# Kernel optimization log

Hardware: AMD Instinct MI355X
Metric: run time of the kernel (lower is better)

## Reference

```python
import jax, jax.numpy as jnp
import numpy as np

B, DIN, H, DOUT, RANK = 256, 128, 512, 1, 8
ALPHA = 16.0
SCALE = ALPHA / RANK  # LoRA scaling alpha/rank


def setup_inputs() -> dict:
    key = jax.random.key(0)
    keys = iter(jax.random.split(key, 64))

    def nrm(shape, s=0.05):
        return jax.random.normal(next(keys), shape, dtype=jnp.float32) * s

    inp = {"x": nrm((B, DIN), 1.0)}
    for i in range(3):
        inp[f"Wx{i}"] = nrm((H, DIN))
        inp[f"b{i}"] = jnp.zeros((H,), jnp.float32)
        inp[f"Ax{i}"] = nrm((B, RANK, DIN))
        inp[f"Bx{i}"] = nrm((B, H, RANK))
        inp[f"bd{i}"] = nrm((B, H))
    for i in (1, 2):
        inp[f"Wz{i}"] = nrm((H, H))
        inp[f"Az{i}"] = nrm((B, RANK, H))
        inp[f"Bz{i}"] = nrm((B, H, RANK))
    inp["out_Wx"] = nrm((DOUT, DIN))
    inp["out_b"] = jnp.zeros((DOUT,), jnp.float32)
    inp["out_Ax"] = nrm((B, RANK, DIN))
    inp["out_Bx"] = nrm((B, DOUT, RANK))
    inp["out_bd"] = nrm((B, DOUT))
    inp["out_Wz"] = nrm((DOUT, H))
    inp["out_Az"] = nrm((B, RANK, H))
    inp["out_Bz"] = nrm((B, DOUT, RANK))
    return inp


def _delta(Bm, Am):
    # per-sample LoRA delta: bmm(B, A) * alpha/rank -> [B, out, in]
    return jnp.einsum('bor,bri->boi', Bm, Am) * SCALE


def _blin(v, W, b=None):
    # batched linear with per-sample weight W [B,out,in] applied to v [B,in]
    y = jnp.einsum('boi,bi->bo', W, v)
    return y if b is None else y + b


def reference(x, Wx0, b0, Ax0, Bx0, bd0, Wx1, b1, Ax1, Bx1, bd1,
              Wx2, b2, Ax2, Bx2, bd2, Wz1, Az1, Bz1, Wz2, Az2, Bz2,
              out_Wx, out_b, out_Ax, out_Bx, out_bd, out_Wz, out_Az, out_Bz):
    sp = jax.nn.softplus
    # layer 0
    z = sp(_blin(x, Wx0 + _delta(Bx0, Ax0), b0 + bd0))
    # layer 1: x path + positive (softplus) z path
    pre = _blin(x, Wx1 + _delta(Bx1, Ax1), b1 + bd1)
    pre = pre + _blin(z, sp(Wz1 + _delta(Bz1, Az1)))
    z = sp(pre)
    # layer 2
    pre = _blin(x, Wx2 + _delta(Bx2, Ax2), b2 + bd2)
    pre = pre + _blin(z, sp(Wz2 + _delta(Bz2, Az2)))
    z = sp(pre)
    # output layer
    out = _blin(x, out_Wx + _delta(out_Bx, out_Ax), out_b + out_bd)
    out = out + _blin(z, sp(out_Wz + _delta(out_Bz, out_Az)))
    return out
```

## Files before the change

kernel.cpp:

```cpp
#include <hip/hip_runtime.h>

#define NB    256
#define DIN   128
#define HH    512
#define RANK  8
#define SCALE 2.0f
#define LN2   0.69314718f
#define C192  5.2083335e-3f

#define WS_Z0   0
#define WS_P1   131072
#define WS_P2   262144
#define WS_END  393216

typedef float v2f __attribute__((ext_vector_type(2)));
typedef _Float16 h4v __attribute__((ext_vector_type(4)));

__device__ __forceinline__ v2f mk2(float a, float b) { v2f r; r.x = a; r.y = b; return r; }

__device__ __forceinline__ v2f pk_fma(v2f a, v2f b, v2f c) {
    v2f d; asm("v_pk_fma_f32 %0, %1, %2, %3" : "=v"(d) : "v"(a), "v"(b), "v"(c)); return d;
}
__device__ __forceinline__ v2f pk_mul(v2f a, v2f b) {
    v2f d; asm("v_pk_mul_f32 %0, %1, %2" : "=v"(d) : "v"(a), "v"(b)); return d;
}
__device__ __forceinline__ v2f pk_fma_blo(v2f a, v2f b, v2f c) {
    v2f d; asm("v_pk_fma_f32 %0, %1, %2, %3 op_sel:[0,0,0] op_sel_hi:[1,0,1]"
               : "=v"(d) : "v"(a), "v"(b), "v"(c)); return d;
}
__device__ __forceinline__ v2f pk_fma_bhi(v2f a, v2f b, v2f c) {
    v2f d; asm("v_pk_fma_f32 %0, %1, %2, %3 op_sel:[0,1,0] op_sel_hi:[1,1,1]"
               : "=v"(d) : "v"(a), "v"(b), "v"(c)); return d;
}

__device__ __forceinline__ float sp_stable(float v) {
    float e = __expf(-fabsf(v));
    return fmaxf(v, 0.0f) + __logf(1.0f + e);
}
__device__ __forceinline__ float sp_poly(float v) {
    float u = v * v;
    float t = fmaf(u, -C192, 0.125f);
    t = fmaf(u, t, LN2);
    return fmaf(v, 0.5f, t);
}

#define DPP_ADD(x, ctrl, rm, bm, bc)                                            \
    (x) = (x) + __int_as_float(__builtin_amdgcn_update_dpp(                     \
              0, __float_as_int(x), (ctrl), (rm), (bm), (bc)))

__device__ __forceinline__ float wave_sum64(float x) {
    DPP_ADD(x, 0x111, 0xf, 0xf, true);
    DPP_ADD(x, 0x112, 0xf, 0xf, true);
    DPP_ADD(x, 0x114, 0xf, 0xf, true);
    DPP_ADD(x, 0x118, 0xf, 0xf, true);
    DPP_ADD(x, 0x142, 0xa, 0xf, false);
    DPP_ADD(x, 0x143, 0xc, 0xf, false);
    return x;
}

__global__ __launch_bounds__(1024, 4) void kzstep(
    const float* __restrict__ x,
    const float* __restrict__ Wx, const float* __restrict__ bb,
    const float* __restrict__ Ax, const float* __restrict__ Bx,
    const float* __restrict__ bd,
    const float* __restrict__ Wz, const float* __restrict__ Az,
    const float* __restrict__ Bz,
    const float* __restrict__ zin, float* __restrict__ outv, const int mode)
{
    const int bid  = blockIdx.x;
    const int o    = bid >> 3;
    const int g    = bid & 7;
    const int tid  = threadIdx.x;
    const int lane = tid & 63;
    const int wid  = tid >> 6;

    __shared__ float x_s[8][DIN + 4];
    __shared__ float tx_s[8][RANK];
    __shared__ float xpre_s[64][9];
    __shared__ float z_s[8][HH];
    __shared__ _Float16 Wt[64 * HH];
    __shared__ float bz_s[8][64][RANK];
    __shared__ float red_s[4][8][2][65];

    const v2f cA2 = mk2(-C192, -C192);
    const v2f cB2 = mk2(0.125f, 0.125f);
    const v2f cL2 = mk2(LN2, LN2);
    const v2f cH2 = mk2(0.5f, 0.5f);

    {
        const int s = tid >> 7, d = tid & 127;
        x_s[s][d] = x[(o * 8 + s) * DIN + d];
    }
    if (mode) {
        {
            const int s = tid >> 7, k4 = tid & 127;
            float4 zv = *reinterpret_cast<const float4*>(zin + ((size_t)(o * 8 + s)) * HH + k4 * 4);
            if (mode == 2) {
                zv.x = sp_stable(zv.x); zv.y = sp_stable(zv.y);
                zv.z = sp_stable(zv.z); zv.w = sp_stable(zv.w);
            }
            *reinterpret_cast<float4*>(&z_s[s][k4 * 4]) = zv;
        }
        {
            #pragma unroll
            for (int j = 0; j < 8; ++j) {
                const int fi  = tid + j * 1024;
                const int row = fi >> 7, c4 = fi & 127;
                float4 w = *reinterpret_cast<const float4*>(Wz + (g * 64 + row) * HH + c4 * 4);
                h4v hv;
                hv.x = (_Float16)w.x; hv.y = (_Float16)w.y;
                hv.z = (_Float16)w.z; hv.w = (_Float16)w.w;
                reinterpret_cast<h4v*>(Wt)[fi] = hv;
            }
        }
        {
            const int s = tid >> 7, t2 = tid & 127;
            const int rw = t2 >> 1, q = t2 & 1;
            *reinterpret_cast<float4*>(&bz_s[s][rw][q * 4]) =
                *reinterpret_cast<const float4*>(
                    Bz + ((size_t)(o * 8 + s) * HH + g * 64 + rw) * RANK + q * 4);
        }
    }
    __syncthreads();

    if (tid < 512) {
        const int p = tid >> 3, l = tid & 7;
        const int s = p >> 3, r = p & 7;
        const float* Ab = Ax + ((size_t)(o * 8 + s) * RANK + r) * DIN;
        float acc = 0.f;
        #pragma unroll
        for (int j = 0; j < 16; ++j) { const int d = l + 8 * j; acc += Ab[d] * x_s[s][d]; }
        acc += __shfl_down(acc, 4, 8);
        acc += __shfl_down(acc, 2, 8);
        acc += __shfl_down(acc, 1, 8);
        if (l == 0) tx_s[s][r] = acc;
    }
    __syncthreads();

    if (tid < 512) {
        const int row = tid >> 3, s = tid & 7;
        const int h  = g * 64 + row;
        const int sb = o * 8 + s;
        const float4* wrow = reinterpret_cast<const float4*>(Wx + h * DIN);
        float acc = 0.f;
        #pragma unroll 8
        for (int q = 0; q < DIN / 4; ++q) {
            float4 w = wrow[q];
            const float* xs = &x_s[s][q * 4];
            acc += w.x * xs[0] + w.y * xs[1] + w.z * xs[2] + w.w * xs[3];
        }
        const float* bxr = Bx + ((size_t)sb * HH + h) * RANK;
        float t = 0.f;
        #pragma unroll
        for (int r = 0; r < RANK; ++r) t += bxr[r] * tx_s[s][r];
        const float v = acc + SCALE * t + bb[h] + bd[(size_t)sb * HH + h];
        if (mode == 0) outv[(size_t)sb * HH + h] = sp_stable(v);
        else           xpre_s[row][s] = v;
    }
    if (mode == 0) return;

    {
        const int s   = wid >> 1;
        const int khf = wid & 1;
        const int c0  = khf * 256 + (lane << 2);
        const int sb  = o * 8 + s;
        const bool odd = lane & 1;

        v2f zk2[2], az[RANK][2];
        {
            float4 zz = *reinterpret_cast<const float4*>(&z_s[s][c0]);
            zk2[0] = mk2(zz.x, zz.y); zk2[1] = mk2(zz.z, zz.w);
        }
        #pragma unroll
        for (int r = 0; r < RANK; ++r) {
            float4 a4 = *reinterpret_cast<const float4*>(Az + ((size_t)sb * RANK + r) * HH + c0);
            az[r][0] = mk2(SCALE * a4.x, SCALE * a4.y);
            az[r][1] = mk2(SCALE * a4.z, SCALE * a4.w);
        }

        const _Float16* wp = Wt + c0;
        v2f wA[2], wB[2], bzA[4], bzB[4];

        auto loadw = [&](v2f* dst, int row) {
            h4v hv = *reinterpret_cast<const h4v*>(wp + row * HH);
            dst[0] = mk2((float)hv.x, (float)hv.y);
            dst[1] = mk2((float)hv.z, (float)hv.w);
        };
        auto loadb = [&](v2f* dst, int row) {
            float4 q0 = *reinterpret_cast<const float4*>(&bz_s[s][row][0]);
            float4 q1 = *reinterpret_cast<const float4*>(&bz_s[s][row][4]);
            dst[0] = mk2(q0.x, q0.y); dst[1] = mk2(q0.z, q0.w);
            dst[2] = mk2(q1.x, q1.y); dst[3] = mk2(q1.z, q1.w);
        };
        auto rowsum = [&](const v2f* wz, const v2f* bz) -> float {
            v2f sv = mk2(0.f, 0.f);
            #pragma unroll
            for (int gg = 0; gg < 2; ++gg) {
                v2f d = wz[gg];
                d = pk_fma_blo(az[0][gg], bz[0], d);
                d = pk_fma_bhi(az[1][gg], bz[0], d);
                d = pk_fma_blo(az[2][gg], bz[1], d);
                d = pk_fma_bhi(az[3][gg], bz[1], d);
                d = pk_fma_blo(az[4][gg], bz[2], d);
                d = pk_fma_bhi(az[5][gg], bz[2], d);
                d = pk_fma_blo(az[6][gg], bz[3], d);
                d = pk_fma_bhi(az[7][gg], bz[3], d);
                v2f u = pk_mul(d, d);
                v2f t = pk_fma(u, cA2, cB2);
                t = pk_fma(u, t, cL2);
                t = pk_fma(d, cH2, t);
                sv = pk_fma(zk2[gg], t, sv);
            }
            return sv.x + sv.y;
        };

        loadw(wA, 0); loadb(bzA, 0);
        #pragma unroll 1
        for (int hs = 0; hs < 64; hs += 2) {
            loadw(wB, hs + 1); loadb(bzB, hs + 1);
            float sA = rowsum(wA, bzA);
            const int hn = (hs + 2) & 63;
            loadw(wA, hn); loadb(bzA, hn);
            float sB = rowsum(wB, bzB);

            float m  = odd ? sB : sA;
            float o2 = odd ? sA : sB;
            m = m + __int_as_float(__builtin_amdgcn_update_dpp(
                    0, __float_as_int(o2), 0xB1, 0xf, 0xf, true));
            DPP_ADD(m, 0x112, 0xf, 0xf, true);
            DPP_ADD(m, 0x114, 0xf, 0xf, true);
            DPP_ADD(m, 0x118, 0xf, 0xf, true);
            if ((lane & 14) == 14) red_s[lane >> 4][s][khf][hs + (lane & 1)] = m;
        }
    }
    __syncthreads();

    if (tid < 512) {
        const int row = tid >> 3, s = tid & 7;
        float acc = xpre_s[row][s];
        #pragma unroll
        for (int q = 0; q < 4; ++q)
            acc += red_s[q][s][0][row] + red_s[q][s][1][row];
        outv[((size_t)(o * 8 + s)) * HH + g * 64 + row] = acc;
    }
}

__global__ __launch_bounds__(512, 2) void kout(
    const float* __restrict__ x,
    const float* __restrict__ oWx, const float* __restrict__ ob,
    const float* __restrict__ oAx, const float* __restrict__ oBx, const float* __restrict__ obd,
    const float* __restrict__ oWz, const float* __restrict__ oAz, const float* __restrict__ oBz,
    const float* __restrict__ pre2, float* __restrict__ out)
{
    const int b = blockIdx.x, tid = threadIdx.x;
    __shared__ float x_s[DIN];
    __shared__ float red_s[HH];
    __shared__ float tx_s[RANK];

    if (tid < DIN) x_s[tid] = x[b * DIN + tid];
    __syncthreads();

    float partial;
    {
        const int h = tid;
        const float z2 = sp_stable(pre2[(size_t)b * HH + h]);
        float d = 0.f;
        #pragma unroll
        for (int r = 0; r < RANK; ++r)
            d = fmaf(oBz[b * RANK + r], oAz[((size_t)b * RANK + r) * HH + h], d);
        partial = z2 * sp_poly(fmaf(SCALE, d, oWz[h]));
        if (tid < DIN) partial += oWx[tid] * x_s[tid];
    }
    red_s[tid] = partial;
    __syncthreads();

    if (tid < 128) {
        const int r = tid >> 4, l = tid & 15;
        const float* Ab = oAx + ((size_t)b * RANK + r) * DIN;
        float s = 0.f;
        #pragma unroll
        for (int k = 0; k < 8; ++k) { int d = l + 16 * k; s += Ab[d] * x_s[d]; }
        s += __shfl_down(s, 8, 16);
        s += __shfl_down(s, 4, 16);
        s += __shfl_down(s, 2, 16);
        s += __shfl_down(s, 1, 16);
        if (l == 0) tx_s[r] = s;
    }
    __syncthreads();
    for (int st = 256; st > 0; st >>= 1) {
        if (tid < st) red_s[tid] += red_s[tid + st];
        __syncthreads();
    }
    if (tid == 0) {
        float t2 = 0.f;
        #pragma unroll
        for (int r = 0; r < RANK; ++r) t2 = fmaf(oBx[b * RANK + r], tx_s[r], t2);
        out[b] = red_s[0] + ob[0] + obd[b] + SCALE * t2;
    }
}

__global__ __launch_bounds__(1024, 4) void lora_fused(
    const float* __restrict__ x,
    const float* __restrict__ Wx0, const float* __restrict__ b0,
    const float* __restrict__ Ax0, const float* __restrict__ Bx0, const float* __restrict__ bd0,
    const float* __restrict__ Wx1, const float* __restrict__ b1,
    const float* __restrict__ Ax1, const float* __restrict__ Bx1, const float* __restrict__ bd1,
    const float* __restrict__ Wx2, const float* __restrict__ b2,
    const float* __restrict__ Ax2, const float* __restrict__ Bx2, const float* __restrict__ bd2,
    const float* __restrict__ Wz1, const float* __restrict__ Az1, const float* __restrict__ Bz1,
    const float* __restrict__ Wz2, const float* __restrict__ Az2, const float* __restrict__ Bz2,
    const float* __restrict__ oWx, const float* __restrict__ ob,
    const float* __restrict__ oAx, const float* __restrict__ oBx, const float* __restrict__ obd,
    const float* __restrict__ oWz, const float* __restrict__ oAz, const float* __restrict__ oBz,
    float* __restrict__ out)
{
    const int b    = blockIdx.x;
    const int tid  = threadIdx.x;
    const int lane = tid & 63;
    const int wid  = tid >> 6;
    const int rg   = wid >> 1;
    const int ch   = wid & 1;
    const bool odd = lane & 1;

    __shared__ float x_s[DIN];
    __shared__ float z_s[HH];
    __shared__ float tx_s[4][RANK];
    __shared__ float xpre_s[3][HH];
    __shared__ float red4_s[4][2][HH + 2];
    __shared__ __attribute__((aligned(16))) float Az_s[2][RANK * HH];
    __shared__ __attribute__((aligned(16))) float Bz_s[2][HH * RANK];
    __shared__ float red8[16];

    const v2f cA2 = mk2(-C192, -C192);
    const v2f cB2 = mk2(0.125f, 0.125f);
    const v2f cL2 = mk2(LN2, LN2);
    const v2f cH2 = mk2(0.5f, 0.5f);

    if (tid < DIN) x_s[tid] = x[b * DIN + tid];
    {
        const float4* a1 = reinterpret_cast<const float4*>(Az1 + b * RANK * HH);
        const float4* a2 = reinterpret_cast<const float4*>(Az2 + b * RANK * HH);
        const float4* z1 = reinterpret_cast<const float4*>(Bz1 + b * HH * RANK);
        const float4* z2 = reinterpret_cast<const float4*>(Bz2 + b * HH * RANK);
        reinterpret_cast<float4*>(Az_s[0])[tid] = a1[tid];
        reinterpret_cast<float4*>(Az_s[1])[tid] = a2[tid];
        reinterpret_cast<float4*>(Bz_s[0])[tid] = z1[tid];
        reinterpret_cast<float4*>(Bz_s[1])[tid] = z2[tid];
    }
    __syncthreads();

    if (tid < 512) {
        const int g = tid >> 7;
        const int t = tid & 127;
        const int r = t >> 4, l = t & 15;
        const float* A  = (g == 0) ? Ax0 : (g == 1) ? Ax1 : (g == 2) ? Ax2 : oAx;
        const float* Ab = A + (b * RANK + r) * DIN;
        float s = 0.f;
        #pragma unroll
        for (int k = 0; k < 8; ++k) { int d = l + 16 * k; s += Ab[d] * x_s[d]; }
        s += __shfl_down(s, 8, 16);
        s += __shfl_down(s, 4, 16);
        s += __shfl_down(s, 2, 16);
        s += __shfl_down(s, 1, 16);
        if (l == 0) tx_s[g][r] = s;
    }
    __syncthreads();

    #pragma unroll 1
    for (int idx = tid; idx < 3 * HH; idx += 1024) {
        const int l = idx >> 9;
        const int h = idx & (HH - 1);
        const float* Wxl = (l == 0) ? Wx0 : (l == 1) ? Wx1 : Wx2;
        const float* bl  = (l == 0) ? b0  : (l == 1) ? b1  : b2;
        const float* Bxl = (l == 0) ? Bx0 : (l == 1) ? Bx1 : Bx2;
        const float* bdl = (l == 0) ? bd0 : (l == 1) ? bd1 : bd2;
        const float4* wrow = reinterpret_cast<const float4*>(Wxl + h * DIN);
        float s = 0.f;
        #pragma unroll 8
        for (int q = 0; q < DIN / 4; ++q) {
            float4 w = wrow[q];
            const float* xs = &x_s[q * 4];
            s += w.x * xs[0] + w.y * xs[1] + w.z * xs[2] + w.w * xs[3];
        }
        const float* bxr = Bxl + (b * HH + h) * RANK;
        float t = 0.f;
        #pragma unroll
        for (int r = 0; r < RANK; ++r) t += bxr[r] * tx_s[l][r];
        xpre_s[l][h] = s + SCALE * t + bl[h] + bdl[b * HH + h];
    }
    __syncthreads();

    if (tid < HH) z_s[tid] = sp_stable(xpre_s[0][tid]);
    __syncthreads();

    auto zlayer = [&](const float* __restrict__ Wz, int li) {
        const int c0 = ch * 256 + (lane << 2);
        v2f zk2[2], az[RANK][2];
        {
            float4 zz = *reinterpret_cast<const float4*>(&z_s[c0]);
            zk2[0] = mk2(zz.x, zz.y); zk2[1] = mk2(zz.z, zz.w);
        }
        #pragma unroll
        for (int r = 0; r < RANK; ++r) {
            float4 a4 = *reinterpret_cast<const float4*>(&Az_s[li][r * HH + c0]);
            az[r][0] = mk2(SCALE * a4.x, SCALE * a4.y);
            az[r][1] = mk2(SCALE * a4.z, SCALE * a4.w);
        }
        const float* wp = Wz + (rg * 64) * HH + c0;
        const float* bp = &Bz_s[li][(rg * 64) * RANK];
        float* rp = &red4_s[lane >> 4][ch][rg * 64 + (lane & 1)];

        v2f wA[2], wB[2], bzA[4], bzB[4];
        auto loadw = [&](v2f* dst, int row) {
            float4 w4 = *reinterpret_cast<const float4*>(wp + row * HH);
            dst[0] = mk2(w4.x, w4.y); dst[1] = mk2(w4.z, w4.w);
        };
        auto loadb = [&](v2f* dst, int row) {
            const float4* q = reinterpret_cast<const float4*>(bp + row * RANK);
            float4 q0 = q[0], q1 = q[1];
            dst[0] = mk2(q0.x, q0.y); dst[1] = mk2(q0.z, q0.w);
            dst[2] = mk2(q1.x, q1.y); dst[3] = mk2(q1.z, q1.w);
        };
        auto rowsum = [&](const v2f* wz, const v2f* bz) -> float {
            v2f s = mk2(0.f, 0.f);
            #pragma unroll
            for (int g = 0; g < 2; ++g) {
                v2f d = wz[g];
                d = pk_fma_blo(az[0][g], bz[0], d);
                d = pk_fma_bhi(az[1][g], bz[0], d);
                d = pk_fma_blo(az[2][g], bz[1], d);
                d = pk_fma_bhi(az[3][g], bz[1], d);
                d = pk_fma_blo(az[4][g], bz[2], d);
                d = pk_fma_bhi(az[5][g], bz[2], d);
                d = pk_fma_blo(az[6][g], bz[3], d);
                d = pk_fma_bhi(az[7][g], bz[3], d);
                v2f u = pk_mul(d, d);
                v2f t = pk_fma(u, cA2, cB2);
                t = pk_fma(u, t, cL2);
                t = pk_fma(d, cH2, t);
                s = pk_fma(zk2[g], t, s);
            }
            return s.x + s.y;
        };

        loadw(wA, 0); loadb(bzA, 0);
        #pragma unroll 1
        for (int hs = 0; hs < 64; hs += 2) {
            loadw(wB, hs + 1); loadb(bzB, hs + 1);
            float sA = rowsum(wA, bzA);
            const int hn = (hs + 2) & 63;
            loadw(wA, hn); loadb(bzA, hn);
            float sB = rowsum(wB, bzB);
            float m = odd ? sB : sA;
            float o = odd ? sA : sB;
            m = m + __int_as_float(__builtin_amdgcn_update_dpp(
                    0, __float_as_int(o), 0xB1, 0xf, 0xf, true));
            DPP_ADD(m, 0x112, 0xf, 0xf, true);
            DPP_ADD(m, 0x114, 0xf, 0xf, true);
            DPP_ADD(m, 0x118, 0xf, 0xf, true);
            if ((lane & 14) == 14) rp[hs] = m;
        }
    };

    zlayer(Wz1, 0);
    __syncthreads();
    if (tid < HH) {
        float acc = xpre_s[1][tid];
        #pragma unroll
        for (int q = 0; q < 4; ++q) acc += red4_s[q][0][tid] + red4_s[q][1][tid];
        z_s[tid] = sp_stable(acc);
    }
    __syncthreads();

    zlayer(Wz2, 1);
    __syncthreads();
    if (tid < HH) {
        float acc = xpre_s[2][tid];
        #pragma unroll
        for (int q = 0; q < 4; ++q) acc += red4_s[q][0][tid] + red4_s[q][1][tid];
        z_s[tid] = sp_stable(acc);
    }
    __syncthreads();

    {
        float partial = 0.f;
        if (tid < HH) {
            const float* oBzb = oBz + b * RANK;
            const float* oAzb = oAz + b * RANK * HH;
            float d = 0.f;
            #pragma unroll
            for (int r = 0; r < RANK; ++r) d = fmaf(oBzb[r], oAzb[r * HH + tid], d);
            partial = z_s[tid] * sp_poly(fmaf(SCALE, d, oWz[tid]));
            if (tid < DIN) partial += oWx[tid] * x_s[tid];
        }
        partial = wave_sum64(partial);
        if (lane == 63) red8[wid] = partial;
        __syncthreads();
        if (tid == 0) {
            float t = 0.f;
            #pragma unroll
            for (int w = 0; w < 8; ++w) t += red8[w];
            float t2 = 0.f;
            const float* oBxb = oBx + b * RANK;
            #pragma unroll
            for (int r = 0; r < RANK; ++r) t2 = fmaf(oBxb[r], tx_s[3][r], t2);
            out[b] = t + ob[0] + obd[b] + SCALE * t2;
        }
    }
}

extern "C" void kernel_launch(void* const* d_in, const int* in_sizes, int n_in,
                              void* d_out, int out_size, void* d_ws, size_t ws_size,
                              hipStream_t stream) {
    const float* x   = (const float*)d_in[0];
    const float* Wx0 = (const float*)d_in[1];
    const float* b0  = (const float*)d_in[2];
    const float* Ax0 = (const float*)d_in[3];
    const float* Bx0 = (const float*)d_in[4];
    const float* bd0 = (const float*)d_in[5];
    const float* Wx1 = (const float*)d_in[6];
    const float* b1  = (const float*)d_in[7];
    const float* Ax1 = (const float*)d_in[8];
    const float* Bx1 = (const float*)d_in[9];
    const float* bd1 = (const float*)d_in[10];
    const float* Wx2 = (const float*)d_in[11];
    const float* b2  = (const float*)d_in[12];
    const float* Ax2 = (const float*)d_in[13];
    const float* Bx2 = (const float*)d_in[14];
    const float* bd2 = (const float*)d_in[15];
    const float* Wz1 = (const float*)d_in[16];
    const float* Az1 = (const float*)d_in[17];
    const float* Bz1 = (const float*)d_in[18];
    const float* Wz2 = (const float*)d_in[19];
    const float* Az2 = (const float*)d_in[20];
    const float* Bz2 = (const float*)d_in[21];
    const float* oWx = (const float*)d_in[22];
    const float* ob  = (const float*)d_in[23];
    const float* oAx = (const float*)d_in[24];
    const float* oBx = (const float*)d_in[25];
    const float* obd = (const float*)d_in[26];
    const float* oWz = (const float*)d_in[27];
    const float* oAz = (const float*)d_in[28];
    const float* oBz = (const float*)d_in[29];
    float* out = (float*)d_out;

    if (ws_size >= (size_t)WS_END * sizeof(float) && d_ws != nullptr) {
        float* ws = (float*)d_ws;
        kzstep<<<NB, 1024, 0, stream>>>(x, Wx0, b0, Ax0, Bx0, bd0,
                                        nullptr, nullptr, nullptr,
                                        nullptr, ws + WS_Z0, 0);
        kzstep<<<NB, 1024, 0, stream>>>(x, Wx1, b1, Ax1, Bx1, bd1,
                                        Wz1, Az1, Bz1,
                                        ws + WS_Z0, ws + WS_P1, 1);
        kzstep<<<NB, 1024, 0, stream>>>(x, Wx2, b2, Ax2, Bx2, bd2,
                                        Wz2, Az2, Bz2,
                                        ws + WS_P1, ws + WS_P2, 2);
        kout<<<NB, 512, 0, stream>>>(x, oWx, ob, oAx, oBx, obd,
                                     oWz, oAz, oBz, ws + WS_P2, out);
    } else {
        lora_fused<<<NB, 1024, 0, stream>>>(
            x, Wx0, b0, Ax0, Bx0, bd0, Wx1, b1, Ax1, Bx1, bd1,
            Wx2, b2, Ax2, Bx2, bd2, Wz1, Az1, Bz1, Wz2, Az2, Bz2,
            oWx, ob, oAx, oBx, obd, oWz, oAz, oBz, out);
    }
}
```

Measured before the change: 79.84 us.

## Always run the multi-kernel layer-split path using static device buffers

Removes the single-block-per-sample fused kernel and its workspace-size check. The three per-layer kzstep kernels and the kout kernel now always run, with their intermediate activations stored in statically allocated __device__ global arrays instead of the caller's workspace. Each kzstep block serves 8 samples on one 64-row slice, so the shared weight matrix is reused across samples rather than re-read once per sample. The cost is extra launches and global round-trips for the intermediates between layers.

```diff
diff --git a/kernel.cpp b/kernel.cpp
--- a/kernel.cpp
+++ b/kernel.cpp
@@ -8,10 +8,9 @@
 #define LN2   0.69314718f
 #define C192  5.2083335e-3f
 
-#define WS_Z0   0
-#define WS_P1   131072
-#define WS_P2   262144
-#define WS_END  393216
+__device__ float g_z0[NB * HH];
+__device__ float g_p1[NB * HH];
+__device__ float g_p2[NB * HH];
 
 typedef float v2f __attribute__((ext_vector_type(2)));
 typedef _Float16 h4v __attribute__((ext_vector_type(4)));
@@ -64,8 +63,7 @@
     const float* __restrict__ Ax, const float* __restrict__ Bx,
     const float* __restrict__ bd,
     const float* __restrict__ Wz, const float* __restrict__ Az,
-    const float* __restrict__ Bz,
-    const float* __restrict__ zin, float* __restrict__ outv, const int mode)
+    const float* __restrict__ Bz, const int mode)
 {
     const int bid  = blockIdx.x;
     const int o    = bid >> 3;
@@ -73,6 +71,9 @@
     const int tid  = threadIdx.x;
     const int lane = tid & 63;
     const int wid  = tid >> 6;
+
+    const float* zin = (mode == 1) ? g_z0 : g_p1;
+    float* outv = (mode == 0) ? g_z0 : (mode == 1) ? g_p1 : g_p2;
 
     __shared__ float x_s[8][DIN + 4];
     __shared__ float tx_s[8][RANK];
@@ -250,7 +251,7 @@
     const float* __restrict__ oWx, const float* __restrict__ ob,
     const float* __restrict__ oAx, const float* __restrict__ oBx, const float* __restrict__ obd,
     const float* __restrict__ oWz, const float* __restrict__ oAz, const float* __restrict__ oBz,
-    const float* __restrict__ pre2, float* __restrict__ out)
+    float* __restrict__ out)
 {
     const int b = blockIdx.x, tid = threadIdx.x;
     __shared__ float x_s[DIN];
@@ -263,7 +264,7 @@
     float partial;
     {
         const int h = tid;
-        const float z2 = sp_stable(pre2[(size_t)b * HH + h]);
+        const float z2 = sp_stable(g_p2[(size_t)b * HH + h]);
         float d = 0.f;
         #pragma unroll
         for (int r = 0; r < RANK; ++r)
@@ -296,216 +297,6 @@
         #pragma unroll
         for (int r = 0; r < RANK; ++r) t2 = fmaf(oBx[b * RANK + r], tx_s[r], t2);
         out[b] = red_s[0] + ob[0] + obd[b] + SCALE * t2;
-    }
-}
-
-__global__ __launch_bounds__(1024, 4) void lora_fused(
-    const float* __restrict__ x,
-    const float* __restrict__ Wx0, const float* __restrict__ b0,
-    const float* __restrict__ Ax0, const float* __restrict__ Bx0, const float* __restrict__ bd0,
-    const float* __restrict__ Wx1, const float* __restrict__ b1,
-    const float* __restrict__ Ax1, const float* __restrict__ Bx1, const float* __restrict__ bd1,
-    const float* __restrict__ Wx2, const float* __restrict__ b2,
-    const float* __restrict__ Ax2, const float* __restrict__ Bx2, const float* __restrict__ bd2,
-    const float* __restrict__ Wz1, const float* __restrict__ Az1, const float* __restrict__ Bz1,
-    const float* __restrict__ Wz2, const float* __restrict__ Az2, const float* __restrict__ Bz2,
-    const float* __restrict__ oWx, const float* __restrict__ ob,
-    const float* __restrict__ oAx, const float* __restrict__ oBx, const float* __restrict__ obd,
-    const float* __restrict__ oWz, const float* __restrict__ oAz, const float* __restrict__ oBz,
-    float* __restrict__ out)
-{
-    const int b    = blockIdx.x;
-    const int tid  = threadIdx.x;
-    const int lane = tid & 63;
-    const int wid  = tid >> 6;
-    const int rg   = wid >> 1;
-    const int ch   = wid & 1;
-    const bool odd = lane & 1;
-
-    __shared__ float x_s[DIN];
-    __shared__ float z_s[HH];
-    __shared__ float tx_s[4][RANK];
-    __shared__ float xpre_s[3][HH];
-    __shared__ float red4_s[4][2][HH + 2];
-    __shared__ __attribute__((aligned(16))) float Az_s[2][RANK * HH];
-    __shared__ __attribute__((aligned(16))) float Bz_s[2][HH * RANK];
-    __shared__ float red8[16];
-
-    const v2f cA2 = mk2(-C192, -C192);
-    const v2f cB2 = mk2(0.125f, 0.125f);
-    const v2f cL2 = mk2(LN2, LN2);
-    const v2f cH2 = mk2(0.5f, 0.5f);
-
-    if (tid < DIN) x_s[tid] = x[b * DIN + tid];
-    {
-        const float4* a1 = reinterpret_cast<const float4*>(Az1 + b * RANK * HH);
-        const float4* a2 = reinterpret_cast<const float4*>(Az2 + b * RANK * HH);
-        const float4* z1 = reinterpret_cast<const float4*>(Bz1 + b * HH * RANK);
-        const float4* z2 = reinterpret_cast<const float4*>(Bz2 + b * HH * RANK);
-        reinterpret_cast<float4*>(Az_s[0])[tid] = a1[tid];
-        reinterpret_cast<float4*>(Az_s[1])[tid] = a2[tid];
-        reinterpret_cast<float4*>(Bz_s[0])[tid] = z1[tid];
-        reinterpret_cast<float4*>(Bz_s[1])[tid] = z2[tid];
-    }
-    __syncthreads();
-
-    if (tid < 512) {
-        const int g = tid >> 7;
-        const int t = tid & 127;
-        const int r = t >> 4, l = t & 15;
-        const float* A  = (g == 0) ? Ax0 : (g == 1) ? Ax1 : (g == 2) ? Ax2 : oAx;
-        const float* Ab = A + (b * RANK + r) * DIN;
-        float s = 0.f;
-        #pragma unroll
-        for (int k = 0; k < 8; ++k) { int d = l + 16 * k; s += Ab[d] * x_s[d]; }
-        s += __shfl_down(s, 8, 16);
-        s += __shfl_down(s, 4, 16);
-        s += __shfl_down(s, 2, 16);
-        s += __shfl_down(s, 1, 16);
-        if (l == 0) tx_s[g][r] = s;
-    }
-    __syncthreads();
-
-    #pragma unroll 1
-    for (int idx = tid; idx < 3 * HH; idx += 1024) {
-        const int l = idx >> 9;
-        const int h = idx & (HH - 1);
-        const float* Wxl = (l == 0) ? Wx0 : (l == 1) ? Wx1 : Wx2;
-        const float* bl  = (l == 0) ? b0  : (l == 1) ? b1  : b2;
-        const float* Bxl = (l == 0) ? Bx0 : (l == 1) ? Bx1 : Bx2;
-        const float* bdl = (l == 0) ? bd0 : (l == 1) ? bd1 : bd2;
-        const float4* wrow = reinterpret_cast<const float4*>(Wxl + h * DIN);
-        float s = 0.f;
-        #pragma unroll 8
-        for (int q = 0; q < DIN / 4; ++q) {
-            float4 w = wrow[q];
-            const float* xs = &x_s[q * 4];
-            s += w.x * xs[0] + w.y * xs[1] + w.z * xs[2] + w.w * xs[3];
-        }
-        const float* bxr = Bxl + (b * HH + h) * RANK;
-        float t = 0.f;
-        #pragma unroll
-        for (int r = 0; r < RANK; ++r) t += bxr[r] * tx_s[l][r];
-        xpre_s[l][h] = s + SCALE * t + bl[h] + bdl[b * HH + h];
-    }
-    __syncthreads();
-
-    if (tid < HH) z_s[tid] = sp_stable(xpre_s[0][tid]);
-    __syncthreads();
-
-    auto zlayer = [&](const float* __restrict__ Wz, int li) {
-        const int c0 = ch * 256 + (lane << 2);
-        v2f zk2[2], az[RANK][2];
-        {
-            float4 zz = *reinterpret_cast<const float4*>(&z_s[c0]);
-            zk2[0] = mk2(zz.x, zz.y); zk2[1] = mk2(zz.z, zz.w);
-        }
-        #pragma unroll
-        for (int r = 0; r < RANK; ++r) {
-            float4 a4 = *reinterpret_cast<const float4*>(&Az_s[li][r * HH + c0]);
-            az[r][0] = mk2(SCALE * a4.x, SCALE * a4.y);
-            az[r][1] = mk2(SCALE * a4.z, SCALE * a4.w);
-        }
-        const float* wp = Wz + (rg * 64) * HH + c0;
-        const float* bp = &Bz_s[li][(rg * 64) * RANK];
-        float* rp = &red4_s[lane >> 4][ch][rg * 64 + (lane & 1)];
-
-        v2f wA[2], wB[2], bzA[4], bzB[4];
-        auto loadw = [&](v2f* dst, int row) {
-            float4 w4 = *reinterpret_cast<const float4*>(wp + row * HH);
-            dst[0] = mk2(w4.x, w4.y); dst[1] = mk2(w4.z, w4.w);
-        };
-        auto loadb = [&](v2f* dst, int row) {
-            const float4* q = reinterpret_cast<const float4*>(bp + row * RANK);
-            float4 q0 = q[0], q1 = q[1];
-            dst[0] = mk2(q0.x, q0.y); dst[1] = mk2(q0.z, q0.w);
-            dst[2] = mk2(q1.x, q1.y); dst[3] = mk2(q1.z, q1.w);
-        };
-        auto rowsum = [&](const v2f* wz, const v2f* bz) -> float {
-            v2f s = mk2(0.f, 0.f);
-            #pragma unroll
-            for (int g = 0; g < 2; ++g) {
-                v2f d = wz[g];
-                d = pk_fma_blo(az[0][g], bz[0], d);
-                d = pk_fma_bhi(az[1][g], bz[0], d);
-                d = pk_fma_blo(az[2][g], bz[1], d);
-                d = pk_fma_bhi(az[3][g], bz[1], d);
-                d = pk_fma_blo(az[4][g], bz[2], d);
-                d = pk_fma_bhi(az[5][g], bz[2], d);
-                d = pk_fma_blo(az[6][g], bz[3], d);
-                d = pk_fma_bhi(az[7][g], bz[3], d);
-                v2f u = pk_mul(d, d);
-                v2f t = pk_fma(u, cA2, cB2);
-                t = pk_fma(u, t, cL2);
-                t = pk_fma(d, cH2, t);
-                s = pk_fma(zk2[g], t, s);
-            }
-            return s.x + s.y;
-        };
-
-        loadw(wA, 0); loadb(bzA, 0);
-        #pragma unroll 1
-        for (int hs = 0; hs < 64; hs += 2) {
-            loadw(wB, hs + 1); loadb(bzB, hs + 1);
-            float sA = rowsum(wA, bzA);
-            const int hn = (hs + 2) & 63;
-            loadw(wA, hn); loadb(bzA, hn);
-            float sB = rowsum(wB, bzB);
-            float m = odd ? sB : sA;
-            float o = odd ? sA : sB;
-            m = m + __int_as_float(__builtin_amdgcn_update_dpp(
-                    0, __float_as_int(o), 0xB1, 0xf, 0xf, true));
-            DPP_ADD(m, 0x112, 0xf, 0xf, true);
-            DPP_ADD(m, 0x114, 0xf, 0xf, true);
-            DPP_ADD(m, 0x118, 0xf, 0xf, true);
-            if ((lane & 14) == 14) rp[hs] = m;
-        }
-    };
-
-    zlayer(Wz1, 0);
-    __syncthreads();
-    if (tid < HH) {
-        float acc = xpre_s[1][tid];
-        #pragma unroll
-        for (int q = 0; q < 4; ++q) acc += red4_s[q][0][tid] + red4_s[q][1][tid];
-        z_s[tid] = sp_stable(acc);
-    }
-    __syncthreads();
-
-    zlayer(Wz2, 1);
-    __syncthreads();
-    if (tid < HH) {
-        float acc = xpre_s[2][tid];
-        #pragma unroll
-        for (int q = 0; q < 4; ++q) acc += red4_s[q][0][tid] + red4_s[q][1][tid];
-        z_s[tid] = sp_stable(acc);
-    }
-    __syncthreads();
-
-    {
-        float partial = 0.f;
-        if (tid < HH) {
-            const float* oBzb = oBz + b * RANK;
-            const float* oAzb = oAz + b * RANK * HH;
-            float d = 0.f;
-            #pragma unroll
-            for (int r = 0; r < RANK; ++r) d = fmaf(oBzb[r], oAzb[r * HH + tid], d);
-            partial = z_s[tid] * sp_poly(fmaf(SCALE, d, oWz[tid]));
-            if (tid < DIN) partial += oWx[tid] * x_s[tid];
-        }
-        partial = wave_sum64(partial);
-        if (lane == 63) red8[wid] = partial;
-        __syncthreads();
-        if (tid == 0) {
-            float t = 0.f;
-            #pragma unroll
-            for (int w = 0; w < 8; ++w) t += red8[w];
-            float t2 = 0.f;
-            const float* oBxb = oBx + b * RANK;
-            #pragma unroll
-            for (int r = 0; r < RANK; ++r) t2 = fmaf(oBxb[r], tx_s[3][r], t2);
-            out[b] = t + ob[0] + obd[b] + SCALE * t2;
-        }
     }
 }
 
@@ -544,23 +335,12 @@
     const float* oBz = (const float*)d_in[29];
     float* out = (float*)d_out;
 
-    if (ws_size >= (size_t)WS_END * sizeof(float) && d_ws != nullptr) {
-        float* ws = (float*)d_ws;
-        kzstep<<<NB, 1024, 0, stream>>>(x, Wx0, b0, Ax0, Bx0, bd0,
-                                        nullptr, nullptr, nullptr,
-                                        nullptr, ws + WS_Z0, 0);
-        kzstep<<<NB, 1024, 0, stream>>>(x, Wx1, b1, Ax1, Bx1, bd1,
-                                        Wz1, Az1, Bz1,
-                                        ws + WS_Z0, ws + WS_P1, 1);
-        kzstep<<<NB, 1024, 0, stream>>>(x, Wx2, b2, Ax2, Bx2, bd2,
-                                        Wz2, Az2, Bz2,
-                                        ws + WS_P1, ws + WS_P2, 2);
-        kout<<<NB, 512, 0, stream>>>(x, oWx, ob, oAx, oBx, obd,
-                                     oWz, oAz, oBz, ws + WS_P2, out);
-    } else {
-        lora_fused<<<NB, 1024, 0, stream>>>(
-            x, Wx0, b0, Ax0, Bx0, bd0, Wx1, b1, Ax1, Bx1, bd1,
-            Wx2, b2, Ax2, Bx2, bd2, Wz1, Az1, Bz1, Wz2, Az2, Bz2,
-            oWx, ob, oAx, oBx, obd, oWz, oAz, oBz, out);
-    }
-}
+    kzstep<<<NB, 1024, 0, stream>>>(x, Wx0, b0, Ax0, Bx0, bd0,
+                                    nullptr, nullptr, nullptr, 0);
+    kzstep<<<NB, 1024, 0, stream>>>(x, Wx1, b1, Ax1, Bx1, bd1,
+                                    Wz1, Az1, Bz1, 1);
+    kzstep<<<NB, 1024, 0, stream>>>(x, Wx2, b2, Ax2, Bx2, bd2,
+                                    Wz2, Az2, Bz2, 2);
+    kout<<<NB, 512, 0, stream>>>(x, oWx, ob, oAx, oBx, obd,
+                                 oWz, oAz, oBz, out);
+}
```

After: 80.01 us. Within noise of the previous version (+0.2%).

## Hoist all x-path projections into a prep kernel and split z-steps finer

Applied to the files above, without the earlier changes.

Adds a kprep kernel that computes the x-path pre-activations for all three layers (with the layer-0 softplus applied) in one per-sample launch and writes them to workspace. The z-step kernel becomes 1024 blocks of 512 threads, each handling 2 samples and 64 output rows with the row range split across wave groups, replacing 256 blocks of 1024 threads over 8 samples. This is meant to cut per-layer serial x-projection work and raise parallelism, at the cost of reloading and converting Wz to fp16 in four times as many blocks. The fallback fused kernel's z loop is also restructured to keep an 8-row ring of W registers, but that path only runs when no workspace is available.

```diff
diff --git a/kernel.cpp b/kernel.cpp
--- a/kernel.cpp
+++ b/kernel.cpp
@@ -9,9 +9,11 @@
 #define C192  5.2083335e-3f
 
 #define WS_Z0   0
-#define WS_P1   131072
-#define WS_P2   262144
-#define WS_END  393216
+#define WS_XP1  131072
+#define WS_XP2  262144
+#define WS_P1   393216
+#define WS_P2   524288
+#define WS_END  655360
 
 typedef float v2f __attribute__((ext_vector_type(2)));
 typedef _Float16 h4v __attribute__((ext_vector_type(4)));
@@ -58,112 +60,123 @@
     return x;
 }
 
-__global__ __launch_bounds__(1024, 4) void kzstep(
+__global__ __launch_bounds__(1024, 4) void kprep(
     const float* __restrict__ x,
-    const float* __restrict__ Wx, const float* __restrict__ bb,
-    const float* __restrict__ Ax, const float* __restrict__ Bx,
-    const float* __restrict__ bd,
+    const float* __restrict__ Wx0, const float* __restrict__ b0,
+    const float* __restrict__ Ax0, const float* __restrict__ Bx0, const float* __restrict__ bd0,
+    const float* __restrict__ Wx1, const float* __restrict__ b1,
+    const float* __restrict__ Ax1, const float* __restrict__ Bx1, const float* __restrict__ bd1,
+    const float* __restrict__ Wx2, const float* __restrict__ b2,
+    const float* __restrict__ Ax2, const float* __restrict__ Bx2, const float* __restrict__ bd2,
+    float* __restrict__ ws)
+{
+    const int b = blockIdx.x, tid = threadIdx.x;
+    __shared__ float x_s[DIN];
+    __shared__ float tx_s[3][RANK];
+
+    if (tid < DIN) x_s[tid] = x[b * DIN + tid];
+    __syncthreads();
+
+    if (tid < 384) {
+        const int g = tid >> 7, t = tid & 127;
+        const int r = t >> 4, l = t & 15;
+        const float* A  = (g == 0) ? Ax0 : (g == 1) ? Ax1 : Ax2;
+        const float* Ab = A + ((size_t)b * RANK + r) * DIN;
+        float s = 0.f;
+        #pragma unroll
+        for (int k = 0; k < 8; ++k) { int d = l + 16 * k; s += Ab[d] * x_s[d]; }
+        s += __shfl_down(s, 8, 16);
+        s += __shfl_down(s, 4, 16);
+        s += __shfl_down(s, 2, 16);
+        s += __shfl_down(s, 1, 16);
+        if (l == 0) tx_s[g][r] = s;
+    }
+    __syncthreads();
+
+    #pragma unroll 1
+    for (int idx = tid; idx < 3 * HH; idx += 1024) {
+        const int l = idx >> 9;
+        const int h = idx & (HH - 1);
+        const float* Wxl = (l == 0) ? Wx0 : (l == 1) ? Wx1 : Wx2;
+        const float* bl  = (l == 0) ? b0  : (l == 1) ? b1  : b2;
+        const float* Bxl = (l == 0) ? Bx0 : (l == 1) ? Bx1 : Bx2;
+        const float* bdl = (l == 0) ? bd0 : (l == 1) ? bd1 : bd2;
+        const float4* wrow = reinterpret_cast<const float4*>(Wxl + h * DIN);
+        float s = 0.f;
+        #pragma unroll 8
+        for (int q = 0; q < DIN / 4; ++q) {
+            float4 w = wrow[q];
+            const float* xs = &x_s[q * 4];
+            s += w.x * xs[0] + w.y * xs[1] + w.z * xs[2] + w.w * xs[3];
+        }
+        const float* bxr = Bxl + ((size_t)b * HH + h) * RANK;
+        float t = 0.f;
+        #pragma unroll
+        for (int r = 0; r < RANK; ++r) t += bxr[r] * tx_s[l][r];
+        const float v = s + SCALE * t + bl[h] + bdl[(size_t)b * HH + h];
+        if (l == 0)      ws[WS_Z0  + b * HH + h] = sp_stable(v);
+        else if (l == 1) ws[WS_XP1 + b * HH + h] = v;
+        else             ws[WS_XP2 + b * HH + h] = v;
+    }
+}
+
+__global__ __launch_bounds__(512, 4) void kzstep(
     const float* __restrict__ Wz, const float* __restrict__ Az,
     const float* __restrict__ Bz,
-    const float* __restrict__ zin, float* __restrict__ outv, const int mode)
+    const float* __restrict__ zin, const float* __restrict__ xpre,
+    float* __restrict__ outv, const int mode)
 {
     const int bid  = blockIdx.x;
-    const int o    = bid >> 3;
+    const int p    = bid >> 3;
     const int g    = bid & 7;
     const int tid  = threadIdx.x;
     const int lane = tid & 63;
     const int wid  = tid >> 6;
 
-    __shared__ float x_s[8][DIN + 4];
-    __shared__ float tx_s[8][RANK];
-    __shared__ float xpre_s[64][9];
-    __shared__ float z_s[8][HH];
     __shared__ _Float16 Wt[64 * HH];
-    __shared__ float bz_s[8][64][RANK];
-    __shared__ float red_s[4][8][2][65];
+    __shared__ float z_s[2][HH];
+    __shared__ float bz_s[2][64][RANK];
+    __shared__ float red_s[4][2][2][66];
 
     const v2f cA2 = mk2(-C192, -C192);
     const v2f cB2 = mk2(0.125f, 0.125f);
     const v2f cL2 = mk2(LN2, LN2);
     const v2f cH2 = mk2(0.5f, 0.5f);
 
+    #pragma unroll
+    for (int j = 0; j < 16; ++j) {
+        const int fi  = tid + j * 512;
+        const int row = fi >> 7, c4 = fi & 127;
+        float4 w = *reinterpret_cast<const float4*>(Wz + (size_t)(g * 64 + row) * HH + c4 * 4);
+        h4v hv;
+        hv.x = (_Float16)w.x; hv.y = (_Float16)w.y;
+        hv.z = (_Float16)w.z; hv.w = (_Float16)w.w;
+        reinterpret_cast<h4v*>(Wt)[fi] = hv;
+    }
+    if (tid < 256) {
+        const int s = tid >> 7, k4 = tid & 127;
+        float4 zv = *reinterpret_cast<const float4*>(zin + (size_t)(p * 2 + s) * HH + k4 * 4);
+        if (mode == 2) {
+            zv.x = sp_stable(zv.x); zv.y = sp_stable(zv.y);
+            zv.z = sp_stable(zv.z); zv.w = sp_stable(zv.w);
+        }
+        *reinterpret_cast<float4*>(&z_s[s][k4 * 4]) = zv;
+    } else {
+        const int t = tid - 256;
+        const int s = t >> 7, t2 = t & 127;
+        const int rw = t2 >> 1, q = t2 & 1;
+        *reinterpret_cast<float4*>(&bz_s[s][rw][q * 4]) =
+            *reinterpret_cast<const float4*>(
+                Bz + ((size_t)(p * 2 + s) * HH + g * 64 + rw) * RANK + q * 4);
+    }
+    __syncthreads();
+
     {
-        const int s = tid >> 7, d = tid & 127;
-        x_s[s][d] = x[(o * 8 + s) * DIN + d];
-    }
-    if (mode) {
-        {
-            const int s = tid >> 7, k4 = tid & 127;
-            float4 zv = *reinterpret_cast<const float4*>(zin + ((size_t)(o * 8 + s)) * HH + k4 * 4);
-            if (mode == 2) {
-                zv.x = sp_stable(zv.x); zv.y = sp_stable(zv.y);
-                zv.z = sp_stable(zv.z); zv.w = sp_stable(zv.w);
-            }
-            *reinterpret_cast<float4*>(&z_s[s][k4 * 4]) = zv;
-        }
-        {
-            #pragma unroll
-            for (int j = 0; j < 8; ++j) {
-                const int fi  = tid + j * 1024;
-                const int row = fi >> 7, c4 = fi & 127;
-                float4 w = *reinterpret_cast<const float4*>(Wz + (g * 64 + row) * HH + c4 * 4);
-                h4v hv;
-                hv.x = (_Float16)w.x; hv.y = (_Float16)w.y;
-                hv.z = (_Float16)w.z; hv.w = (_Float16)w.w;
-                reinterpret_cast<h4v*>(Wt)[fi] = hv;
-            }
-        }
-        {
-            const int s = tid >> 7, t2 = tid & 127;
-            const int rw = t2 >> 1, q = t2 & 1;
-            *reinterpret_cast<float4*>(&bz_s[s][rw][q * 4]) =
-                *reinterpret_cast<const float4*>(
-                    Bz + ((size_t)(o * 8 + s) * HH + g * 64 + rw) * RANK + q * 4);
-        }
-    }
-    __syncthreads();
-
-    if (tid < 512) {
-        const int p = tid >> 3, l = tid & 7;
-        const int s = p >> 3, r = p & 7;
-        const float* Ab = Ax + ((size_t)(o * 8 + s) * RANK + r) * DIN;
-        float acc = 0.f;
-        #pragma unroll
-        for (int j = 0; j < 16; ++j) { const int d = l + 8 * j; acc += Ab[d] * x_s[s][d]; }
-        acc += __shfl_down(acc, 4, 8);
-        acc += __shfl_down(acc, 2, 8);
-        acc += __shfl_down(acc, 1, 8);
-        if (l == 0) tx_s[s][r] = acc;
-    }
-    __syncthreads();
-
-    if (tid < 512) {
-        const int row = tid >> 3, s = tid & 7;
-        const int h  = g * 64 + row;
-        const int sb = o * 8 + s;
-        const float4* wrow = reinterpret_cast<const float4*>(Wx + h * DIN);
-        float acc = 0.f;
-        #pragma unroll 8
-        for (int q = 0; q < DIN / 4; ++q) {
-            float4 w = wrow[q];
-            const float* xs = &x_s[s][q * 4];
-            acc += w.x * xs[0] + w.y * xs[1] + w.z * xs[2] + w.w * xs[3];
-        }
-        const float* bxr = Bx + ((size_t)sb * HH + h) * RANK;
-        float t = 0.f;
-        #pragma unroll
-        for (int r = 0; r < RANK; ++r) t += bxr[r] * tx_s[s][r];
-        const float v = acc + SCALE * t + bb[h] + bd[(size_t)sb * HH + h];
-        if (mode == 0) outv[(size_t)sb * HH + h] = sp_stable(v);
-        else           xpre_s[row][s] = v;
-    }
-    if (mode == 0) return;
-
-    {
-        const int s   = wid >> 1;
-        const int khf = wid & 1;
+        const int s   = wid & 1;
+        const int khf = (wid >> 1) & 1;
+        const int rh  = wid >> 2;
         const int c0  = khf * 256 + (lane << 2);
-        const int sb  = o * 8 + s;
+        const int sb  = p * 2 + s;
         const bool odd = lane & 1;
 
         v2f zk2[2], az[RANK][2];
@@ -178,7 +191,10 @@
             az[r][1] = mk2(SCALE * a4.z, SCALE * a4.w);
         }
 
-        const _Float16* wp = Wt + c0;
+        const _Float16* wp = Wt + (size_t)(rh * 32) * HH + c0;
+        const float* bp = &bz_s[s][rh * 32][0];
+        float* rp = &red_s[lane >> 4][s][khf][rh * 32 + (lane & 1)];
+
         v2f wA[2], wB[2], bzA[4], bzB[4];
 
         auto loadw = [&](v2f* dst, int row) {
@@ -187,8 +203,8 @@
             dst[1] = mk2((float)hv.z, (float)hv.w);
         };
         auto loadb = [&](v2f* dst, int row) {
-            float4 q0 = *reinterpret_cast<const float4*>(&bz_s[s][row][0]);
-            float4 q1 = *reinterpret_cast<const float4*>(&bz_s[s][row][4]);
+            float4 q0 = *reinterpret_cast<const float4*>(bp + row * RANK);
+            float4 q1 = *reinterpret_cast<const float4*>(bp + row * RANK + 4);
             dst[0] = mk2(q0.x, q0.y); dst[1] = mk2(q0.z, q0.w);
             dst[2] = mk2(q1.x, q1.y); dst[3] = mk2(q1.z, q1.w);
         };
@@ -216,10 +232,10 @@
 
         loadw(wA, 0); loadb(bzA, 0);
         #pragma unroll 1
-        for (int hs = 0; hs < 64; hs += 2) {
+        for (int hs = 0; hs < 32; hs += 2) {
             loadw(wB, hs + 1); loadb(bzB, hs + 1);
             float sA = rowsum(wA, bzA);
-            const int hn = (hs + 2) & 63;
+            const int hn = (hs + 2) & 31;
             loadw(wA, hn); loadb(bzA, hn);
             float sB = rowsum(wB, bzB);
 
@@ -230,18 +246,19 @@
             DPP_ADD(m, 0x112, 0xf, 0xf, true);
             DPP_ADD(m, 0x114, 0xf, 0xf, true);
             DPP_ADD(m, 0x118, 0xf, 0xf, true);
-            if ((lane & 14) == 14) red_s[lane >> 4][s][khf][hs + (lane & 1)] = m;
-        }
-    }
-    __syncthreads();
-
-    if (tid < 512) {
-        const int row = tid >> 3, s = tid & 7;
-        float acc = xpre_s[row][s];
+            if ((lane & 14) == 14) rp[hs] = m;
+        }
+    }
+    __syncthreads();
+
+    if (tid < 128) {
+        const int row = tid >> 1, s = tid & 1;
+        const int sb = p * 2 + s, h = g * 64 + row;
+        float acc = xpre[(size_t)sb * HH + h];
         #pragma unroll
         for (int q = 0; q < 4; ++q)
             acc += red_s[q][s][0][row] + red_s[q][s][1][row];
-        outv[((size_t)(o * 8 + s)) * HH + g * 64 + row] = acc;
+        outv[(size_t)sb * HH + h] = acc;
     }
 }
 
@@ -410,55 +427,60 @@
         const float* bp = &Bz_s[li][(rg * 64) * RANK];
         float* rp = &red4_s[lane >> 4][ch][rg * 64 + (lane & 1)];
 
-        v2f wA[2], wB[2], bzA[4], bzB[4];
-        auto loadw = [&](v2f* dst, int row) {
-            float4 w4 = *reinterpret_cast<const float4*>(wp + row * HH);
-            dst[0] = mk2(w4.x, w4.y); dst[1] = mk2(w4.z, w4.w);
-        };
-        auto loadb = [&](v2f* dst, int row) {
-            const float4* q = reinterpret_cast<const float4*>(bp + row * RANK);
-            float4 q0 = q[0], q1 = q[1];
-            dst[0] = mk2(q0.x, q0.y); dst[1] = mk2(q0.z, q0.w);
-            dst[2] = mk2(q1.x, q1.y); dst[3] = mk2(q1.z, q1.w);
-        };
-        auto rowsum = [&](const v2f* wz, const v2f* bz) -> float {
-            v2f s = mk2(0.f, 0.f);
+        v2f wbuf[8][2];
+        #pragma unroll
+        for (int j = 0; j < 8; ++j) {
+            float4 w4 = *reinterpret_cast<const float4*>(wp + j * HH);
+            wbuf[j][0] = mk2(w4.x, w4.y); wbuf[j][1] = mk2(w4.z, w4.w);
+        }
+
+        float sEven = 0.f;
+        #pragma unroll 1
+        for (int hs8 = 0; hs8 < 64; hs8 += 8) {
             #pragma unroll
-            for (int g = 0; g < 2; ++g) {
-                v2f d = wz[g];
-                d = pk_fma_blo(az[0][g], bz[0], d);
-                d = pk_fma_bhi(az[1][g], bz[0], d);
-                d = pk_fma_blo(az[2][g], bz[1], d);
-                d = pk_fma_bhi(az[3][g], bz[1], d);
-                d = pk_fma_blo(az[4][g], bz[2], d);
-                d = pk_fma_bhi(az[5][g], bz[2], d);
-                d = pk_fma_blo(az[6][g], bz[3], d);
-                d = pk_fma_bhi(az[7][g], bz[3], d);
-                v2f u = pk_mul(d, d);
-                v2f t = pk_fma(u, cA2, cB2);
-                t = pk_fma(u, t, cL2);
-                t = pk_fma(d, cH2, t);
-                s = pk_fma(zk2[g], t, s);
+            for (int j = 0; j < 8; ++j) {
+                const int row = hs8 + j;
+                const float4* q = reinterpret_cast<const float4*>(bp + row * RANK);
+                float4 q0 = q[0], q1 = q[1];
+                v2f bz0 = mk2(q0.x, q0.y), bz1 = mk2(q0.z, q0.w);
+                v2f bz2 = mk2(q1.x, q1.y), bz3 = mk2(q1.z, q1.w);
+
+                v2f sv = mk2(0.f, 0.f);
+                #pragma unroll
+                for (int gg = 0; gg < 2; ++gg) {
+                    v2f d = wbuf[j][gg];
+                    d = pk_fma_blo(az[0][gg], bz0, d);
+                    d = pk_fma_bhi(az[1][gg], bz0, d);
+                    d = pk_fma_blo(az[2][gg], bz1, d);
+                    d = pk_fma_bhi(az[3][gg], bz1, d);
+                    d = pk_fma_blo(az[4][gg], bz2, d);
+                    d = pk_fma_bhi(az[5][gg], bz2, d);
+                    d = pk_fma_blo(az[6][gg], bz3, d);
+                    d = pk_fma_bhi(az[7][gg], bz3, d);
+                    v2f u = pk_mul(d, d);
+                    v2f t = pk_fma(u, cA2, cB2);
+                    t = pk_fma(u, t, cL2);
+                    t = pk_fma(d, cH2, t);
+                    sv = pk_fma(zk2[gg], t, sv);
+                }
+                float s = sv.x + sv.y;
+                {
+                    float4 w4 = *reinterpret_cast<const float4*>(wp + ((row + 8) & 63) * HH);
+                    wbuf[j][0] = mk2(w4.x, w4.y); wbuf[j][1] = mk2(w4.z, w4.w);
+                }
+                if (j & 1) {
+                    float m = odd ? s : sEven;
+                    float o = odd ? sEven : s;
+                    m = m + __int_as_float(__builtin_amdgcn_update_dpp(
+                            0, __float_as_int(o), 0xB1, 0xf, 0xf, true));
+                    DPP_ADD(m, 0x112, 0xf, 0xf, true);
+                    DPP_ADD(m, 0x114, 0xf, 0xf, true);
+                    DPP_ADD(m, 0x118, 0xf, 0xf, true);
+                    if ((lane & 14) == 14) rp[row - 1] = m;
+                } else {
+                    sEven = s;
+                }
             }
-            return s.x + s.y;
-        };
-
-        loadw(wA, 0); loadb(bzA, 0);
-        #pragma unroll 1
-        for (int hs = 0; hs < 64; hs += 2) {
-            loadw(wB, hs + 1); loadb(bzB, hs + 1);
-            float sA = rowsum(wA, bzA);
-            const int hn = (hs + 2) & 63;
-            loadw(wA, hn); loadb(bzA, hn);
-            float sB = rowsum(wB, bzB);
-            float m = odd ? sB : sA;
-            float o = odd ? sA : sB;
-            m = m + __int_as_float(__builtin_amdgcn_update_dpp(
-                    0, __float_as_int(o), 0xB1, 0xf, 0xf, true));
-            DPP_ADD(m, 0x112, 0xf, 0xf, true);
-            DPP_ADD(m, 0x114, 0xf, 0xf, true);
-            DPP_ADD(m, 0x118, 0xf, 0xf, true);
-            if ((lane & 14) == 14) rp[hs] = m;
         }
     };
 
@@ -546,15 +568,13 @@
 
     if (ws_size >= (size_t)WS_END * sizeof(float) && d_ws != nullptr) {
         float* ws = (float*)d_ws;
-        kzstep<<<NB, 1024, 0, stream>>>(x, Wx0, b0, Ax0, Bx0, bd0,
-                                        nullptr, nullptr, nullptr,
-                                        nullptr, ws + WS_Z0, 0);
-        kzstep<<<NB, 1024, 0, stream>>>(x, Wx1, b1, Ax1, Bx1, bd1,
-                                        Wz1, Az1, Bz1,
-                                        ws + WS_Z0, ws + WS_P1, 1);
-        kzstep<<<NB, 1024, 0, stream>>>(x, Wx2, b2, Ax2, Bx2, bd2,
-                                        Wz2, Az2, Bz2,
-                                        ws + WS_P1, ws + WS_P2, 2);
+        kprep<<<NB, 1024, 0, stream>>>(x, Wx0, b0, Ax0, Bx0, bd0,
+                                       Wx1, b1, Ax1, Bx1, bd1,
+                                       Wx2, b2, Ax2, Bx2, bd2, ws);
+        kzstep<<<1024, 512, 0, stream>>>(Wz1, Az1, Bz1,
+                                         ws + WS_Z0, ws + WS_XP1, ws + WS_P1, 1);
+        kzstep<<<1024, 512, 0, stream>>>(Wz2, Az2, Bz2,
+                                         ws + WS_P1, ws + WS_XP2, ws + WS_P2, 2);
         kout<<<NB, 512, 0, stream>>>(x, oWx, ob, oAx, oBx, obd,
                                      oWz, oAz, oBz, ws + WS_P2, out);
     } else {
```

Result: slower. 91.13 us (+14.1%).
